# Kernel tuning notes

Hardware: AMD Instinct MI355X
Metric: run time of the kernel (lower is better)

## Reference

```python
import jax, jax.numpy as jnp
import numpy as np

N_INIT = jnp.array([17.047, 14.099, 3.625], dtype=jnp.float32)
CA_INIT = jnp.array([16.967, 12.784, 4.338], dtype=jnp.float32)
C_INIT = jnp.array([15.685, 12.755, 5.133], dtype=jnp.float32)


def _unit(x):
    return x / (jnp.linalg.norm(x, axis=-1, keepdims=True) + 1e-8)


def _place_dihedral(a, b, c, bond_angle, bond_length, torsion):
    # a,b,c: [B,3]; bond_angle/bond_length/torsion: [B]
    ab = b - a
    bc = _unit(c - b)
    cr = jnp.cross(ab, bc)
    crn = jnp.linalg.norm(cr, axis=-1, keepdims=True)
    n_main = _unit(cr)
    # collinear fallback (per-element; almost never triggers for real angles)
    perp = jnp.zeros_like(bc).at[..., 0].set(1.0)
    ct = jnp.cross(bc, perp)
    ctn = jnp.linalg.norm(ct, axis=-1, keepdims=True)
    perp2 = jnp.where(ctn < 1e-6, jnp.zeros_like(bc).at[..., 1].set(1.0), perp)
    n_fb = _unit(jnp.cross(bc, perp2))
    n = jnp.where(crn < 1e-6, n_fb, n_main)
    nbc = jnp.cross(n, bc)
    m = jnp.stack([bc, nbc, n], axis=-1)  # [B,3,3]
    d_local = jnp.stack([
        -bond_length * jnp.cos(bond_angle),
        bond_length * jnp.cos(torsion) * jnp.sin(bond_angle),
        bond_length * jnp.sin(torsion) * jnp.sin(bond_angle),
    ], axis=-1)  # [B,3]
    d = jnp.einsum('bij,bj->bi', m, d_local)
    return d + c


def _nerf_build(phi, psi, omega, bond_lengths, bond_angles):
    B, L = phi.shape
    init = jnp.broadcast_to(jnp.stack([N_INIT, CA_INIT, C_INIT]), (B, 3, 3))
    # per-step params, leading axis = residue index i in [0, L-2]
    xs = (
        psi[:, :L - 1].T,                 # psi_i
        omega[:, :L - 1].T,               # omega_i
        phi[:, 1:].T,                     # phi_{i+1}
        bond_lengths[:, :L - 1, 2].T,     # C-N length
        bond_lengths[:, :L - 1, 0].T,     # N-CA length
        bond_lengths[:, :L - 1, 1].T,     # CA-C length
        bond_angles[:, :L - 1, 1].T,      # CA-C-N angle
        bond_angles[:, :L - 1, 2].T,      # C-N-CA angle
        bond_angles[:, :L - 1, 0].T,      # N-CA-C angle
    )

    def step(prev, x):
        psi_i, omega_i, phi_i, len_cn, len_nca, len_cac, ang_cacn, ang_cnca, ang_ncac = x
        a, b, c = prev[:, 0], prev[:, 1], prev[:, 2]
        n = _place_dihedral(a, b, c, ang_cacn, len_cn, psi_i)
        ca = _place_dihedral(b, c, n, ang_cnca, len_nca, omega_i)
        cc = _place_dihedral(c, n, ca, ang_ncac, len_cac, phi_i)
        new = jnp.stack([n, ca, cc], axis=1)  # [B,3,3]
        return new, new

    _, outs = jax.lax.scan(step, init, xs)  # [L-1,B,3,3]
    rest = outs.transpose(1, 0, 2, 3).reshape(B, 3 * (L - 1), 3)
    return jnp.concatenate([init, rest], axis=1)  # [B, 3L, 3]


def setup_inputs() -> dict:
    key = jax.random.key(0)
    k0, k1, k2, k3, k4 = jax.random.split(key, 5)
    B, L = 4096, 512
    phi = jax.random.normal(k0, (B, L), dtype=jnp.float32)
    psi = jax.random.normal(k1, (B, L), dtype=jnp.float32)
    omega = jax.random.normal(k2, (B, L), dtype=jnp.float32)
    # realistic positive bond lengths (~1.0-1.5 A) and bond angles (~1.5-2.3 rad)
    bond_lengths = 1.0 + 0.5 * jax.random.uniform(k3, (B, L, 3), dtype=jnp.float32)
    bond_angles = 1.5 + 0.8 * jax.random.uniform(k4, (B, L, 3), dtype=jnp.float32)
    return {"phi": phi, "psi": psi, "omega": omega,
            "bond_lengths": bond_lengths, "bond_angles": bond_angles}


def reference(phi, psi, omega, bond_lengths, bond_angles):
    return _nerf_build(phi, psi, omega, bond_lengths, bond_angles)
```

## Files before the change

### kernel.cpp

```cpp
#include <hip/hip_runtime.h>
#include <math.h>


#define LCH 512

struct Xf { float r[9]; float t[3]; };

__device__ __forceinline__ Xf xf_compose(const Xf& A, const Xf& B) {
  Xf C;
#pragma unroll
  for (int i = 0; i < 3; ++i) {
    float a0 = A.r[3*i+0], a1 = A.r[3*i+1], a2 = A.r[3*i+2];
    C.r[3*i+0] = a0*B.r[0] + a1*B.r[3] + a2*B.r[6];
    C.r[3*i+1] = a0*B.r[1] + a1*B.r[4] + a2*B.r[7];
    C.r[3*i+2] = a0*B.r[2] + a1*B.r[5] + a2*B.r[8];
    C.t[i]     = a0*B.t[0] + a1*B.t[1] + a2*B.t[2] + A.t[i];
  }
  return C;
}

__device__ __forceinline__ void xf_step(Xf& P, float theta, float len, float tau) {
  float st, ct, sx, cx;
  __sincosf(theta, &st, &ct);
  __sincosf(tau, &sx, &cx);
  float ux = -ct, uy = cx*st, uz = sx*st;
  float v0 = -st, v1 = -ct*cx, v2 = -ct*sx;
  float c00 = P.r[0]*ux + P.r[1]*uy + P.r[2]*uz;
  float c10 = P.r[3]*ux + P.r[4]*uy + P.r[5]*uz;
  float c20 = P.r[6]*ux + P.r[7]*uy + P.r[8]*uz;
  float c01 = P.r[0]*v0 + P.r[1]*v1 + P.r[2]*v2;
  float c11 = P.r[3]*v0 + P.r[4]*v1 + P.r[5]*v2;
  float c21 = P.r[6]*v0 + P.r[7]*v1 + P.r[8]*v2;
  float c02 = P.r[2]*cx - P.r[1]*sx;
  float c12 = P.r[5]*cx - P.r[4]*sx;
  float c22 = P.r[8]*cx - P.r[7]*sx;
  P.t[0] += len*c00; P.t[1] += len*c10; P.t[2] += len*c20;
  P.r[0]=c00; P.r[1]=c01; P.r[2]=c02;
  P.r[3]=c10; P.r[4]=c11; P.r[5]=c12;
  P.r[6]=c20; P.r[7]=c21; P.r[8]=c22;
}

__device__ __forceinline__ void xf_set_delta(Xf& P, float theta, float len, float tau) {
  float st, ct, sx, cx;
  __sincosf(theta, &st, &ct);
  __sincosf(tau, &sx, &cx);
  float ux = -ct, uy = cx*st, uz = sx*st;
  P.r[0]=ux; P.r[1]=-st;    P.r[2]=0.f;
  P.r[3]=uy; P.r[4]=-ct*cx; P.r[5]=-sx;
  P.r[6]=uz; P.r[7]=-ct*sx; P.r[8]=cx;
  P.t[0]=len*ux; P.t[1]=len*uy; P.t[2]=len*uz;
}

__device__ __forceinline__ void xf_identity(Xf& A) {
  A.r[0]=1.f; A.r[1]=0.f; A.r[2]=0.f;
  A.r[3]=0.f; A.r[4]=1.f; A.r[5]=0.f;
  A.r[6]=0.f; A.r[7]=0.f; A.r[8]=1.f;
  A.t[0]=0.f; A.t[1]=0.f; A.t[2]=0.f;
}

__device__ __forceinline__ Xf xf_shfl_up(const Xf& P, int d) {
  Xf O;
#pragma unroll
  for (int i = 0; i < 9; ++i) O.r[i] = __shfl_up(P.r[i], d, 64);
#pragma unroll
  for (int i = 0; i < 3; ++i) O.t[i] = __shfl_up(P.t[i], d, 64);
  return O;
}

#define CSTEP(P, m, k, ax, ay, az) do { \
    float th_, ln_, ta_; \
    if      ((k) == 0) { th_ = BA[3*(m)+1]; ln_ = BL[3*(m)+2]; ta_ = PS[m]; } \
    else if ((k) == 1) { th_ = BA[3*(m)+2]; ln_ = BL[3*(m)+0]; ta_ = OM[m]; } \
    else               { th_ = BA[3*(m)+0]; ln_ = BL[3*(m)+1]; ta_ = PH[m]; } \
    if ((k) == 0) xf_set_delta(P, th_, ln_, ta_); \
    else          xf_step(P, th_, ln_, ta_); \
    ax[k] = P.t[0]; ay[k] = P.t[1]; az[k] = P.t[2]; \
  } while (0)

#define REPF(f) (AP[(f)/9].r[3*((f)%3)+0]*px[(f)/9][((f)%9)/3] \
               + AP[(f)/9].r[3*((f)%3)+1]*py[(f)/9][((f)%9)/3] \
               + AP[(f)/9].r[3*((f)%3)+2]*pz[(f)/9][((f)%9)/3] \
               + AP[(f)/9].t[(f)%3])

__global__ __launch_bounds__(128) void nerf_r16_kernel(
    const float* __restrict__ g_phi, const float* __restrict__ g_psi,
    const float* __restrict__ g_omg, const float* __restrict__ g_bl,
    const float* __restrict__ g_ba, float* __restrict__ g_out)
{
  __shared__ float s_tot[12];
  __shared__ float s_out[4608];

  const int t    = threadIdx.x;
  const int lane = t & 63;
  const int wave = t >> 6;
  const int chain = blockIdx.x;

  const float* phir = g_phi + (size_t)chain * LCH;
  const float* psir = g_psi + (size_t)chain * LCH;
  const float* omgr = g_omg + (size_t)chain * LCH;
  const float* blr  = g_bl  + (size_t)chain * (LCH*3);
  const float* bar  = g_ba  + (size_t)chain * (LCH*3);

  const int j4  = 4 * t;
  const int b12 = 12 * t;

  float4 vps = *(const float4*)(psir + j4);
  float4 vom = *(const float4*)(omgr + j4);
  float4 vph = *(const float4*)(phir + j4);
  float4 l0  = *(const float4*)(blr + b12);
  float4 l1  = *(const float4*)(blr + b12 + 4);
  float4 l2  = *(const float4*)(blr + b12 + 8);
  float4 a0  = *(const float4*)(bar + b12);
  float4 a1  = *(const float4*)(bar + b12 + 4);
  float4 a2  = *(const float4*)(bar + b12 + 8);

  float psN  = __shfl_up(vps.w, 1, 64);
  float omN  = __shfl_up(vom.w, 1, 64);
  float blN0 = __shfl_up(l2.y, 1, 64);
  float blN1 = __shfl_up(l2.z, 1, 64);
  float blN2 = __shfl_up(l2.w, 1, 64);
  float baN0 = __shfl_up(a2.y, 1, 64);
  float baN1 = __shfl_up(a2.z, 1, 64);
  float baN2 = __shfl_up(a2.w, 1, 64);
  if (lane == 0 && t != 0) {
    psN  = psir[j4 - 1];
    omN  = omgr[j4 - 1];
    blN0 = blr[b12 - 3]; blN1 = blr[b12 - 2]; blN2 = blr[b12 - 1];
    baN0 = bar[b12 - 3]; baN1 = bar[b12 - 2]; baN2 = bar[b12 - 1];
  }

  float PS[4] = { psN, vps.x, vps.y, vps.z };
  float OM[4] = { omN, vom.x, vom.y, vom.z };
  float PH[4] = { vph.x, vph.y, vph.z, vph.w };
  float BL[12] = { blN0, blN1, blN2, l0.x, l0.y, l0.z, l0.w,
                   l1.x, l1.y, l1.z, l1.w, l2.x };
  float BA[12] = { baN0, baN1, baN2, a0.x, a0.y, a0.z, a0.w,
                   a1.x, a1.y, a1.z, a1.w, a2.x };

  Xf P0, P1, P2, P3;
  float px[4][3], py[4][3], pz[4][3];
#pragma unroll
  for (int k = 0; k < 3; ++k) {
    CSTEP(P0, 0, k, px[0], py[0], pz[0]);
    CSTEP(P1, 1, k, px[1], py[1], pz[1]);
    CSTEP(P2, 2, k, px[2], py[2], pz[2]);
    CSTEP(P3, 3, k, px[3], py[3], pz[3]);
  }
  if (t == 0) xf_identity(P0);

  Xf P01 = xf_compose(P0, P1);
  Xf P23 = xf_compose(P2, P3);
  Xf P   = xf_compose(P01, P23);

#pragma unroll
  for (int d = 1; d < 64; d <<= 1) {
    Xf O = xf_shfl_up(P, d);
    if (lane >= d) P = xf_compose(O, P);
  }

  if (wave == 0 && lane == 63) {
#pragma unroll
    for (int i = 0; i < 9; ++i) s_tot[i] = P.r[i];
#pragma unroll
    for (int i = 0; i < 3; ++i) s_tot[9+i] = P.t[i];
  }
  Xf E = xf_shfl_up(P, 1);
  __syncthreads();

  Xf A;
  {
    const float ax=17.047f, ay=14.099f, az=3.625f;
    const float bx_=16.967f, by_=12.784f, bz_=4.338f;
    const float cx_=15.685f, cy_=12.755f, cz_=5.133f;
    float abx=bx_-ax, aby=by_-ay, abz=bz_-az;
    float vx=cx_-bx_, vy=cy_-by_, vz=cz_-bz_;
    float vn = sqrtf(vx*vx+vy*vy+vz*vz) + 1e-8f;
    vx/=vn; vy/=vn; vz/=vn;
    float crx = aby*vz - abz*vy;
    float cry = abz*vx - abx*vz;
    float crz = abx*vy - aby*vx;
    float cn = sqrtf(crx*crx+cry*cry+crz*crz) + 1e-8f;
    float nx=crx/cn, ny=cry/cn, nz=crz/cn;
    float mx = ny*vz - nz*vy;
    float my = nz*vx - nx*vz;
    float mz = nx*vy - ny*vx;
    A.r[0]=vx; A.r[1]=mx; A.r[2]=nx;
    A.r[3]=vy; A.r[4]=my; A.r[5]=ny;
    A.r[6]=vz; A.r[7]=mz; A.r[8]=nz;
    A.t[0]=cx_; A.t[1]=cy_; A.t[2]=cz_;
  }
  if (wave == 1) {
    Xf T;
#pragma unroll
    for (int i = 0; i < 9; ++i) T.r[i] = s_tot[i];
#pragma unroll
    for (int i = 0; i < 3; ++i) T.t[i] = s_tot[9+i];
    A = xf_compose(A, T);
  }
  if (lane > 0) A = xf_compose(A, E);

  Xf AP[4];
  AP[0] = A;
  AP[1] = xf_compose(A, P0);
  AP[2] = xf_compose(A, P01);
  AP[3] = xf_compose(AP[2], P2);

#pragma unroll
  for (int q = 0; q < 9; ++q) {
    float4 v;
    v.x = REPF(4*q + 0);
    v.y = REPF(4*q + 1);
    v.z = REPF(4*q + 2);
    v.w = REPF(4*q + 3);
    if (t == 0) {
      if (q == 0) { v.x=17.047f; v.y=14.099f; v.z=3.625f;  v.w=16.967f; }
      if (q == 1) { v.x=12.784f; v.y=4.338f;  v.z=15.685f; v.w=12.755f; }
      if (q == 2) { v.x=5.133f; }
    }
    *(float4*)(s_out + 36*t + 4*q) = v;
  }
  __syncthreads();

  float* orow = g_out + (size_t)chain * 4608;
#pragma unroll
  for (int p = 0; p < 9; ++p) {
    const int g = 512*p + 4*t;
    float4 v = *(const float4*)(s_out + g);
    *(float4*)(orow + g) = v;
  }
}

extern "C" void kernel_launch(void* const* d_in, const int* in_sizes, int n_in,
                              void* d_out, int out_size, void* d_ws, size_t ws_size,
                              hipStream_t stream) {
  const float* phi = (const float*)d_in[0];
  const float* psi = (const float*)d_in[1];
  const float* omg = (const float*)d_in[2];
  const float* bl  = (const float*)d_in[3];
  const float* ba  = (const float*)d_in[4];
  float* out = (float*)d_out;
  const int B = in_sizes[0] / LCH;
  hipLaunchKernelGGL(nerf_r16_kernel, dim3(B), dim3(128), 0, stream,
                     phi, psi, omg, bl, ba, out);
}
```

Baseline: 143.9 us.

## Write outputs directly to global, drop LDS staging, roll scan loop

Removes the 18KB shared-memory output staging buffer and its extra barrier, so each thread writes its 36 contiguous floats straight to global memory as float4 stores. Freeing the LDS can raise the number of blocks resident per CU. The cost is that global stores are no longer coalesced across the wave: each thread now writes a 144-byte strided run. It also keeps the wave-scan loop rolled to cut register pressure, and hardcodes the initial frame matrix as constants.

```diff
diff --git a/kernel.cpp b/kernel.cpp
--- a/kernel.cpp
+++ b/kernel.cpp
@@ -82,13 +82,12 @@
                + AP[(f)/9].r[3*((f)%3)+2]*pz[(f)/9][((f)%9)/3] \
                + AP[(f)/9].t[(f)%3])
 
-__global__ __launch_bounds__(128) void nerf_r16_kernel(
+__global__ __launch_bounds__(128) void nerf_r17_kernel(
     const float* __restrict__ g_phi, const float* __restrict__ g_psi,
     const float* __restrict__ g_omg, const float* __restrict__ g_bl,
     const float* __restrict__ g_ba, float* __restrict__ g_out)
 {
   __shared__ float s_tot[12];
-  __shared__ float s_out[4608];
 
   const int t    = threadIdx.x;
   const int lane = t & 63;
@@ -152,7 +151,7 @@
   Xf P23 = xf_compose(P2, P3);
   Xf P   = xf_compose(P01, P23);
 
-#pragma unroll
+#pragma unroll 1
   for (int d = 1; d < 64; d <<= 1) {
     Xf O = xf_shfl_up(P, d);
     if (lane >= d) P = xf_compose(O, P);
@@ -168,27 +167,10 @@
   __syncthreads();
 
   Xf A;
-  {
-    const float ax=17.047f, ay=14.099f, az=3.625f;
-    const float bx_=16.967f, by_=12.784f, bz_=4.338f;
-    const float cx_=15.685f, cy_=12.755f, cz_=5.133f;
-    float abx=bx_-ax, aby=by_-ay, abz=bz_-az;
-    float vx=cx_-bx_, vy=cy_-by_, vz=cz_-bz_;
-    float vn = sqrtf(vx*vx+vy*vy+vz*vz) + 1e-8f;
-    vx/=vn; vy/=vn; vz/=vn;
-    float crx = aby*vz - abz*vy;
-    float cry = abz*vx - abx*vz;
-    float crz = abx*vy - aby*vx;
-    float cn = sqrtf(crx*crx+cry*cry+crz*crz) + 1e-8f;
-    float nx=crx/cn, ny=cry/cn, nz=crz/cn;
-    float mx = ny*vz - nz*vy;
-    float my = nz*vx - nx*vz;
-    float mz = nx*vy - ny*vx;
-    A.r[0]=vx; A.r[1]=mx; A.r[2]=nx;
-    A.r[3]=vy; A.r[4]=my; A.r[5]=ny;
-    A.r[6]=vz; A.r[7]=mz; A.r[8]=nz;
-    A.t[0]=cx_; A.t[1]=cy_; A.t[2]=cz_;
-  }
+  A.r[0]=-0.849699f; A.r[1]=-0.223843f; A.r[2]=-0.477398f;
+  A.r[3]=-0.019221f; A.r[4]= 0.917962f; A.r[5]=-0.396206f;
+  A.r[6]= 0.526919f; A.r[7]=-0.327477f; A.r[8]=-0.784291f;
+  A.t[0]=15.685f; A.t[1]=12.755f; A.t[2]=5.133f;
   if (wave == 1) {
     Xf T;
 #pragma unroll
@@ -205,6 +187,7 @@
   AP[2] = xf_compose(A, P01);
   AP[3] = xf_compose(AP[2], P2);
 
+  float* orow = g_out + (size_t)chain * 4608 + 36 * t;
 #pragma unroll
   for (int q = 0; q < 9; ++q) {
     float4 v;
@@ -217,16 +200,7 @@
       if (q == 1) { v.x=12.784f; v.y=4.338f;  v.z=15.685f; v.w=12.755f; }
       if (q == 2) { v.x=5.133f; }
     }
-    *(float4*)(s_out + 36*t + 4*q) = v;
-  }
-  __syncthreads();
-
-  float* orow = g_out + (size_t)chain * 4608;
-#pragma unroll
-  for (int p = 0; p < 9; ++p) {
-    const int g = 512*p + 4*t;
-    float4 v = *(const float4*)(s_out + g);
-    *(float4*)(orow + g) = v;
+    *(float4*)(orow + 4*q) = v;
   }
 }
 
@@ -240,6 +214,6 @@
   const float* ba  = (const float*)d_in[4];
   float* out = (float*)d_out;
   const int B = in_sizes[0] / LCH;
-  hipLaunchKernelGGL(nerf_r16_kernel, dim3(B), dim3(128), 0, stream,
+  hipLaunchKernelGGL(nerf_r17_kernel, dim3(B), dim3(128), 0, stream,
                      phi, psi, omg, bl, ba, out);
 }
```

After: 158.1 us. 1.1x slower.
